# Kernel optimization log

Hardware: AMD Instinct MI355X
Metric: run time of the kernel (lower is better)

Reference implementation:

```python
import jax, jax.numpy as jnp
import numpy as np
import math

D_MODEL = 1024
NUM_HEADS = 16


def setup_inputs() -> dict:
    key = jax.random.key(0)
    kx, kq, kk, kv, ko = jax.random.split(key, 5)
    std = math.sqrt(2.0 / (D_MODEL + D_MODEL))
    def w(k):
        return (jax.random.truncated_normal(k, -3.0, 3.0, (D_MODEL, D_MODEL), jnp.float32) * std)
    return {
        "x": jax.random.normal(kx, (2, 2048, D_MODEL), jnp.float32),
        "Wq": w(kq),
        "Wk": w(kk),
        "Wv": w(kv),
        "Wo": w(ko),
    }


def reference(x, Wq, Wk, Wv, Wo):
    B, S, D = x.shape
    H = NUM_HEADS
    dh = D // H
    # projections: weight is (d_out, d_in)
    def proj(t, W):
        y = jnp.einsum('bsd,ed->bse', t, W)
        return y.reshape(B, S, H, dh).transpose(0, 2, 1, 3)  # b h s dh
    Q = proj(x, Wq)
    K = proj(x, Wk)
    V = proj(x, Wv)
    scale = 1.0 / math.sqrt(dh)
    logits = jnp.einsum('bhqd,bhkd->bhqk', Q, K) * scale
    mask = jnp.tril(jnp.ones((S, S), dtype=bool))  # causal
    logits = jnp.where(mask, logits, -jnp.inf)
    weights = jax.nn.softmax(logits, axis=-1)
    attn = jnp.einsum('bhqk,bhkd->bhqd', weights, V)
    attn = attn.transpose(0, 2, 1, 3).reshape(B, S, D)
    return jnp.einsum('bsd,ed->bse', attn, Wo)
```

## Files before the change

kernel.cpp:

```cpp
#include <hip/hip_runtime.h>
#include <hip/hip_bf16.h>

typedef __bf16 bf16x8 __attribute__((ext_vector_type(8)));
typedef float  f32x4  __attribute__((ext_vector_type(4)));
typedef float  f32x16 __attribute__((ext_vector_type(16)));
typedef unsigned short u16x8 __attribute__((ext_vector_type(8)));
typedef unsigned short u16x4 __attribute__((ext_vector_type(4)));
typedef unsigned int   u32x4 __attribute__((ext_vector_type(4)));

#define WAITV(N) asm volatile("s_waitcnt vmcnt(" #N ")" ::: "memory")
#define SBAR()   do { __builtin_amdgcn_s_barrier(); asm volatile("" ::: "memory"); } while (0)


__device__ __forceinline__ unsigned short f2bf(float f) {
  return __builtin_bit_cast(unsigned short, (__bf16)f);
}

__device__ __forceinline__ bf16x8 ld8(const unsigned short* p) {
  return __builtin_bit_cast(bf16x8, *reinterpret_cast<const u16x8*>(p));
}

__device__ __forceinline__ unsigned int cvtpk(float a, float b) {
  unsigned int r;
  asm("v_cvt_pk_bf16_f32 %0, %1, %2" : "=v"(r) : "v"(a), "v"(b));
  return r;
}

__device__ __forceinline__ float e2(float x) {
  float r;
  asm("v_exp_f32 %0, %1" : "=v"(r) : "v"(x));
  return r;
}

__device__ __forceinline__ void gload16(const unsigned short* src, unsigned short* lds) {
  __builtin_amdgcn_global_load_lds(
      (const __attribute__((address_space(1))) unsigned int*)src,
      (__attribute__((address_space(3))) unsigned int*)lds,
      16, 0, 0);
}


__global__ __launch_bounds__(256) void cvt_inputs(
    const float* __restrict__ x, const float* __restrict__ Wq,
    const float* __restrict__ Wk, const float* __restrict__ Wv,
    const float* __restrict__ Wo,
    unsigned short* __restrict__ xb, unsigned short* __restrict__ wb) {
  const int NXC = 4194304 / 8;
  const int NWC = 1048576 / 8;
  const int total = NXC + 4 * NWC;
  for (int cid = blockIdx.x * 256 + threadIdx.x; cid < total; cid += gridDim.x * 256) {
    const float* s; unsigned short* d; int off;
    if (cid < NXC) { s = x; d = xb; off = cid * 8; }
    else {
      const int c2 = cid - NXC; const int w = c2 >> 17; const int o2 = c2 & (NWC - 1);
      s = (w == 0) ? Wq : (w == 1) ? Wk : (w == 2) ? Wv : Wo;
      d = wb + (size_t)w * 1048576;
      off = o2 * 8;
    }
    const f32x4 a  = *reinterpret_cast<const f32x4*>(s + off);
    const f32x4 b2 = *reinterpret_cast<const f32x4*>(s + off + 4);
    u16x8 o;
#pragma unroll
    for (int j = 0; j < 4; ++j) { o[j] = f2bf(a[j]); o[j + 4] = f2bf(b2[j]); }
    *reinterpret_cast<u16x8*>(d + off) = o;
  }
}


template<int BM>
__device__ __forceinline__ void gemm_body(const unsigned short* __restrict__ A,
                                          const unsigned short* __restrict__ W,
                                          void* __restrict__ Cv, int mode) {
  constexpr int FM  = BM / 32;
  constexpr int WTM = BM / 2;
  __shared__ unsigned short As[2][BM * 64];
  __shared__ unsigned short Bs[2][64 * 64];
  const int tid  = threadIdx.x;
  const int lane = tid & 63;
  const int g    = lane >> 4;
  const int lo   = lane & 15;
  const int wid  = tid >> 6;
  const int m0   = blockIdx.y * BM;
  const int n0   = blockIdx.x * 64;
  const int wm   = wid >> 1, wn = wid & 1;

  f32x4 acc[FM][2] = {};

  auto stage = [&](int buf, int k0) {
#pragma unroll
    for (int i = 0; i < BM / 32; ++i) {
      const int c   = i * 256 + tid;
      const int row = c >> 3, cc = c & 7;
      const int scc = cc ^ (row & 7);
      gload16(A + (size_t)(m0 + row) * 1024 + k0 + scc * 8, &As[buf][(i * 4 + wid) * 512]);
    }
#pragma unroll
    for (int i = 0; i < 2; ++i) {
      const int c   = i * 256 + tid;
      const int row = c >> 3, cc = c & 7;
      const int scc = cc ^ (row & 7);
      gload16(W + (size_t)(n0 + row) * 1024 + k0 + scc * 8, &Bs[buf][(i * 4 + wid) * 512]);
    }
  };

  stage(0, 0);
  stage(1, 64);
  int cur = 0;
  for (int t = 0; t < 16; ++t) {
    if (t < 15) {
      if constexpr (BM == 64) WAITV(4); else WAITV(6);
    } else {
      WAITV(0);
    }
    SBAR();
#pragma unroll
    for (int ks = 0; ks < 2; ++ks) {
      const int slot = (ks * 4 + g) ^ (lo & 7);
      bf16x8 af[FM], bvf[2];
#pragma unroll
      for (int mi = 0; mi < FM; ++mi)
        af[mi] = ld8(&As[cur][(wm * WTM + mi * 16 + lo) * 64 + slot * 8]);
#pragma unroll
      for (int ni = 0; ni < 2; ++ni)
        bvf[ni] = ld8(&Bs[cur][(wn * 32 + ni * 16 + lo) * 64 + slot * 8]);
#pragma unroll
      for (int mi = 0; mi < FM; ++mi)
#pragma unroll
        for (int ni = 0; ni < 2; ++ni)
          acc[mi][ni] = __builtin_amdgcn_mfma_f32_16x16x32_bf16(af[mi], bvf[ni], acc[mi][ni], 0, 0, 0);
    }
    SBAR();
    if (t + 2 < 16) stage(cur, (t + 2) * 64);
    cur ^= 1;
  }

#pragma unroll
  for (int mi = 0; mi < FM; ++mi) {
#pragma unroll
    for (int ni = 0; ni < 2; ++ni) {
      const int gcol = n0 + wn * 32 + ni * 16 + lo;
      if (mode == 2) {
        const int s0 = m0 + wm * WTM + mi * 16 + g * 4;
        const int b = s0 >> 11, s = s0 & 2047;
        const int h = gcol >> 6, d = gcol & 63;
        u16x4 pk;
#pragma unroll
        for (int r = 0; r < 4; ++r) pk[r] = f2bf(acc[mi][ni][r]);
        *reinterpret_cast<u16x4*>(
            &((unsigned short*)Cv)[(((size_t)(b * 16 + h)) * 64 + d) * 2048 + s]) = pk;
      } else {
#pragma unroll
        for (int r = 0; r < 4; ++r) {
          const int grow = m0 + wm * WTM + mi * 16 + g * 4 + r;
          if (mode == 0) {
            ((float*)Cv)[(size_t)grow * 1024 + gcol] = acc[mi][ni][r];
          } else {
            const unsigned short bv = f2bf(acc[mi][ni][r]);
            const int b = grow >> 11, s = grow & 2047;
            const int h = gcol >> 6, d = gcol & 63;
            ((unsigned short*)Cv)[(((size_t)(b * 16 + h)) * 2048 + s) * 64 + d] = bv;
          }
        }
      }
    }
  }
}

__global__ __launch_bounds__(256) void gemm_qkv(
    const unsigned short* __restrict__ xb,
    const unsigned short* __restrict__ wb,
    unsigned short* __restrict__ q_s,
    unsigned short* __restrict__ k_s,
    unsigned short* __restrict__ vt_s) {
  const unsigned short* W = wb + (size_t)blockIdx.z * 1048576;
  void* o; int mode;
  if (blockIdx.z == 0)      { o = q_s;  mode = 1; }
  else if (blockIdx.z == 1) { o = k_s;  mode = 1; }
  else                      { o = vt_s; mode = 2; }
  gemm_body<64>(xb, W, o, mode);
}

__global__ __launch_bounds__(256) void gemm_out(
    const unsigned short* __restrict__ a_s,
    const unsigned short* __restrict__ wb,
    float* __restrict__ out) {
  gemm_body<64>(a_s, wb + (size_t)3 * 1048576, out, 0);
}


__global__ __launch_bounds__(512, 4) void attn_fwd(
    const unsigned short* __restrict__ Q,
    const unsigned short* __restrict__ K,
    const unsigned short* __restrict__ Vt,
    unsigned short* __restrict__ O) {
  __shared__ unsigned short Kl[2][128 * 64];
  __shared__ unsigned short Vl[2][2][64 * 64];
  const int tid  = threadIdx.x;
  const int lane = tid & 63;
  const int wid  = tid >> 6;
  const int qs   = wid & 3;
  const int kh   = wid >> 2;
  const int q31  = lane & 31;
  const int hi   = lane >> 5;
  const int bi   = blockIdx.x;
  const int bh   = bi & 31;
  const int j    = (bi < 256) ? (15 - (bi >> 5)) : ((bi - 256) >> 5);
  const int b    = bh >> 4, h = bh & 15;

  const unsigned short* Qb = Q  + (size_t)bh * 2048 * 64;
  const unsigned short* Kb = K  + (size_t)bh * 2048 * 64;
  const unsigned short* Vb = Vt + (size_t)bh * 64 * 2048;
  const float SC = 0.125f * 1.4426950408889634f;

  auto stage = [&](int buf, int t) {
#pragma unroll
    for (int i = 0; i < 2; ++i) {
      const int c   = i * 512 + tid;
      const int row = c >> 3, cc = c & 7;
      const int scc = cc ^ (row & 7);
      gload16(Kb + (size_t)(t * 128 + row) * 64 + scc * 8, &Kl[buf][(i * 8 + wid) * 512]);
    }
#pragma unroll
    for (int i = 0; i < 2; ++i) {
      const int d  = tid >> 3, cc = tid & 7;
      const int scc = cc ^ (d & 7);
      gload16(Vb + (size_t)d * 2048 + t * 128 + i * 64 + scc * 8, &Vl[buf][i][wid * 512]);
    }
  };

  const int R  = j + 1;
  const int qv = j * 128 + qs * 32 + q31;

  bf16x8 qf[4];
#pragma unroll
  for (int ds = 0; ds < 4; ++ds) {
    bf16x8 tq = ld8(Qb + (size_t)qv * 64 + ds * 16 + hi * 8);
#pragma unroll
    for (int jx = 0; jx < 8; ++jx) tq[jx] = (__bf16)((float)tq[jx] * SC);
    qf[ds] = tq;
  }

  f32x16 oacc[2] = {};
  float m = -1.0e30f;
  float l = 0.f;

  stage(0, 0);
  int buf = 0;

  for (int t = 0; t < R; ++t) {
    SBAR();
    if (t + 1 < R) { stage(buf ^ 1, t + 1); WAITV(4); }
    else WAITV(0);
    SBAR();

    const bool lastt = (t == j);
    const bool skipw = lastt && (kh == 1) && (qs < 2);
    if (!skipw) {
      f32x16 sv[2];
      __builtin_amdgcn_s_setprio(1);
#pragma unroll
      for (int kt2 = 0; kt2 < 2; ++kt2) {
        const int row = kh * 64 + kt2 * 32 + q31;
        f32x16 a = {};
#pragma unroll
        for (int ds = 0; ds < 4; ++ds) {
          bf16x8 kf = ld8(&Kl[buf][row * 64 + ((ds * 2 + hi) ^ (row & 7)) * 8]);
          a = __builtin_amdgcn_mfma_f32_32x32x16_bf16(kf, qf[ds], a, 0, 0, 0);
        }
        sv[kt2] = a;
      }
      __builtin_amdgcn_s_setprio(0);

      const bool domask = lastt && !(kh == 0 && qs >= 2);
      float t0 = -1.0e30f, t1 = -1.0e30f, t2 = -1.0e30f, t3 = -1.0e30f;
      if (domask) {
#pragma unroll
        for (int kt2 = 0; kt2 < 2; ++kt2)
#pragma unroll
          for (int r = 0; r < 16; ++r) {
            float v = sv[kt2][r];
            const int key = t * 128 + kh * 64 + kt2 * 32 + (r & 3) + 8 * (r >> 2) + 4 * hi;
            if (key > qv) v = -INFINITY;
            sv[kt2][r] = v;
            if ((r & 3) == 0) t0 = fmaxf(t0, v);
            else if ((r & 3) == 1) t1 = fmaxf(t1, v);
            else if ((r & 3) == 2) t2 = fmaxf(t2, v);
            else t3 = fmaxf(t3, v);
          }
      } else {
#pragma unroll
        for (int kt2 = 0; kt2 < 2; ++kt2)
#pragma unroll
          for (int r = 0; r < 16; ++r) {
            const float v = sv[kt2][r];
            if ((r & 3) == 0) t0 = fmaxf(t0, v);
            else if ((r & 3) == 1) t1 = fmaxf(t1, v);
            else if ((r & 3) == 2) t2 = fmaxf(t2, v);
            else t3 = fmaxf(t3, v);
          }
      }
      const float tmax = fmaxf(fmaxf(t0, t1), fmaxf(t2, t3));

      if (!__all(tmax <= m + 8.f)) {
        float rmax = fmaxf(tmax, __shfl_xor(tmax, 32));
        const float mn   = fmaxf(m, rmax);
        const float corr = e2(m - mn);
        l *= corr;
#pragma unroll
        for (int dt = 0; dt < 2; ++dt)
#pragma unroll
          for (int r = 0; r < 16; ++r) oacc[dt][r] *= corr;
        m = mn;
      }

      float p0 = 0.f, p1 = 0.f, p2 = 0.f, p3 = 0.f;
#pragma unroll
      for (int kt2 = 0; kt2 < 2; ++kt2)
#pragma unroll
        for (int r = 0; r < 16; ++r) {
          const float p = e2(sv[kt2][r] - m);
          sv[kt2][r] = p;
          if ((r & 3) == 0) p0 += p;
          else if ((r & 3) == 1) p1 += p;
          else if ((r & 3) == 2) p2 += p;
          else p3 += p;
        }
      l += (p0 + p1) + (p2 + p3);

      unsigned int pw[4][4];
#pragma unroll
      for (int ks = 0; ks < 4; ++ks) {
        const int kt2 = ks >> 1, Rr = (ks & 1) * 8;
        unsigned int a0 = cvtpk(sv[kt2][Rr + 0], sv[kt2][Rr + 1]);
        unsigned int c0 = cvtpk(sv[kt2][Rr + 4], sv[kt2][Rr + 5]);
        unsigned int a1 = cvtpk(sv[kt2][Rr + 2], sv[kt2][Rr + 3]);
        unsigned int c1 = cvtpk(sv[kt2][Rr + 6], sv[kt2][Rr + 7]);
        asm("v_permlane32_swap_b32 %0, %1" : "+v"(a0), "+v"(c0));
        asm("v_permlane32_swap_b32 %0, %1" : "+v"(a1), "+v"(c1));
        pw[ks][0] = a0; pw[ks][1] = a1; pw[ks][2] = c0; pw[ks][3] = c1;
      }

      __builtin_amdgcn_s_setprio(1);
#pragma unroll
      for (int dt = 0; dt < 2; ++dt) {
        const int dl = dt * 32 + q31;
#pragma unroll
        for (int ks = 0; ks < 4; ++ks) {
          bf16x8 vfr = ld8(&Vl[buf][kh][dl * 64 + ((ks * 2 + hi) ^ (dl & 7)) * 8]);
          u32x4 t4 = {pw[ks][0], pw[ks][1], pw[ks][2], pw[ks][3]};
          bf16x8 pb = __builtin_bit_cast(bf16x8, t4);
          oacc[dt] = __builtin_amdgcn_mfma_f32_32x32x16_bf16(vfr, pb, oacc[dt], 0, 0, 0);
        }
      }
      __builtin_amdgcn_s_setprio(0);
    }

    buf ^= 1;
  }

  SBAR();
  float* VlF = (float*)&Vl[0][0][0];
  float* KlF = (float*)&Kl[0][0];
  const int mi = qs * 64 + lane;
  if (kh == 1) {
    *reinterpret_cast<f32x16*>(&VlF[mi * 32])      = oacc[0];
    *reinterpret_cast<f32x16*>(&VlF[mi * 32 + 16]) = oacc[1];
    KlF[mi * 2] = m; KlF[mi * 2 + 1] = l;
  }
  SBAR();
  if (kh == 0) {
    const f32x16 o1a = *reinterpret_cast<const f32x16*>(&VlF[mi * 32]);
    const f32x16 o1b = *reinterpret_cast<const f32x16*>(&VlF[mi * 32 + 16]);
    const float m1 = KlF[mi * 2], l1 = KlF[mi * 2 + 1];
    const float mm = fmaxf(m, m1);
    const float c0 = e2(m - mm), c1 = e2(m1 - mm);
    float lr = l * c0 + l1 * c1;
    lr += __shfl_xor(lr, 32);
    const float inv = 1.f / lr;
    const size_t obase = ((size_t)(b * 2048 + qv)) * 1024 + h * 64;
#pragma unroll
    for (int dt = 0; dt < 2; ++dt)
#pragma unroll
      for (int r4 = 0; r4 < 4; ++r4) {
        u16x4 pk;
#pragma unroll
        for (int e = 0; e < 4; ++e) {
          const int r = r4 * 4 + e;
          const float o1 = (dt == 0) ? o1a[r] : o1b[r];
          pk[e] = f2bf((oacc[dt][r] * c0 + o1 * c1) * inv);
        }
        *reinterpret_cast<u16x4*>(&O[obase + dt * 32 + r4 * 8 + hi * 4]) = pk;
      }
  }
}


extern "C" void kernel_launch(void* const* d_in, const int* in_sizes, int n_in,
                              void* d_out, int out_size, void* d_ws, size_t ws_size,
                              hipStream_t stream) {
  const float* x  = (const float*)d_in[0];
  const float* Wq = (const float*)d_in[1];
  const float* Wk = (const float*)d_in[2];
  const float* Wv = (const float*)d_in[3];
  const float* Wo = (const float*)d_in[4];
  float* out = (float*)d_out;

  char* ws = (char*)d_ws;
  const size_t MiB = 1024 * 1024;
  unsigned short* x_bf = (unsigned short*)(ws);
  unsigned short* a_s  = (unsigned short*)(ws);
  unsigned short* w_bf = (unsigned short*)(ws + 8  * MiB);
  unsigned short* q_s  = (unsigned short*)(ws + 16 * MiB);
  unsigned short* k_s  = (unsigned short*)(ws + 24 * MiB);
  unsigned short* vt_s = (unsigned short*)(ws + 32 * MiB);

  cvt_inputs<<<2048, dim3(256), 0, stream>>>(x, Wq, Wk, Wv, Wo, x_bf, w_bf);
  gemm_qkv<<<dim3(16, 64, 3), dim3(256), 0, stream>>>(x_bf, w_bf, q_s, k_s, vt_s);
  attn_fwd<<<512, dim3(512), 0, stream>>>(q_s, k_s, vt_s, a_s);
  gemm_out<<<dim3(16, 64, 1), dim3(256), 0, stream>>>(a_s, w_bf, out);
}
```

Baseline: 105.0 us.

## Enlarge projection GEMM tiles and switch to 32x32x16 MFMA with BK=32

Reworks the projection GEMMs to use larger block tiles (128x128 for QKV, 64x128 for output) with a K-step of 32 and the 32x32x16 bf16 MFMA. LDS layout and swizzle are changed to match, and the epilogue is remapped for the 32x32 accumulator layout. The goal is more data reuse per load and fewer LDS reads per MFMA. In exchange there are fewer blocks, twice as many K iterations with barriers, and more accumulator registers per thread.

After: 99.85 us. 4.9% less time.

```diff
diff --git a/kernel.cpp b/kernel.cpp
--- a/kernel.cpp
+++ b/kernel.cpp
@@ -67,91 +67,97 @@
 }
 
 
-template<int BM>
+template<int BM, int BN>
 __device__ __forceinline__ void gemm_body(const unsigned short* __restrict__ A,
                                           const unsigned short* __restrict__ W,
                                           void* __restrict__ Cv, int mode) {
-  constexpr int FM  = BM / 32;
+  constexpr int FM2 = BM / 64;
+  constexpr int NF2 = BN / 64;
   constexpr int WTM = BM / 2;
-  __shared__ unsigned short As[2][BM * 64];
-  __shared__ unsigned short Bs[2][64 * 64];
+  constexpr int WTN = BN / 2;
+  __shared__ unsigned short As[2][BM * 32];
+  __shared__ unsigned short Bs[2][BN * 32];
   const int tid  = threadIdx.x;
   const int lane = tid & 63;
-  const int g    = lane >> 4;
-  const int lo   = lane & 15;
+  const int q31  = lane & 31;
+  const int hi   = lane >> 5;
   const int wid  = tid >> 6;
   const int m0   = blockIdx.y * BM;
-  const int n0   = blockIdx.x * 64;
+  const int n0   = blockIdx.x * BN;
   const int wm   = wid >> 1, wn = wid & 1;
 
-  f32x4 acc[FM][2] = {};
+  f32x16 acc[FM2][NF2] = {};
 
   auto stage = [&](int buf, int k0) {
 #pragma unroll
-    for (int i = 0; i < BM / 32; ++i) {
+    for (int i = 0; i < BM / 64; ++i) {
       const int c   = i * 256 + tid;
-      const int row = c >> 3, cc = c & 7;
-      const int scc = cc ^ (row & 7);
+      const int row = c >> 2, cc = c & 3;
+      const int scc = cc ^ ((row >> 1) & 3);
       gload16(A + (size_t)(m0 + row) * 1024 + k0 + scc * 8, &As[buf][(i * 4 + wid) * 512]);
     }
 #pragma unroll
-    for (int i = 0; i < 2; ++i) {
+    for (int i = 0; i < BN / 64; ++i) {
       const int c   = i * 256 + tid;
-      const int row = c >> 3, cc = c & 7;
-      const int scc = cc ^ (row & 7);
+      const int row = c >> 2, cc = c & 3;
+      const int scc = cc ^ ((row >> 1) & 3);
       gload16(W + (size_t)(n0 + row) * 1024 + k0 + scc * 8, &Bs[buf][(i * 4 + wid) * 512]);
     }
   };
 
   stage(0, 0);
-  stage(1, 64);
+  stage(1, 32);
   int cur = 0;
-  for (int t = 0; t < 16; ++t) {
-    if (t < 15) {
-      if constexpr (BM == 64) WAITV(4); else WAITV(6);
+  for (int t = 0; t < 32; ++t) {
+    if (t < 31) {
+      if constexpr (BM / 64 + BN / 64 == 4) WAITV(4); else WAITV(3);
     } else {
       WAITV(0);
     }
     SBAR();
 #pragma unroll
     for (int ks = 0; ks < 2; ++ks) {
-      const int slot = (ks * 4 + g) ^ (lo & 7);
-      bf16x8 af[FM], bvf[2];
-#pragma unroll
-      for (int mi = 0; mi < FM; ++mi)
-        af[mi] = ld8(&As[cur][(wm * WTM + mi * 16 + lo) * 64 + slot * 8]);
-#pragma unroll
-      for (int ni = 0; ni < 2; ++ni)
-        bvf[ni] = ld8(&Bs[cur][(wn * 32 + ni * 16 + lo) * 64 + slot * 8]);
-#pragma unroll
-      for (int mi = 0; mi < FM; ++mi)
-#pragma unroll
-        for (int ni = 0; ni < 2; ++ni)
-          acc[mi][ni] = __builtin_amdgcn_mfma_f32_16x16x32_bf16(af[mi], bvf[ni], acc[mi][ni], 0, 0, 0);
+      const int slot = (2 * ks + hi) ^ ((q31 >> 1) & 3);
+      bf16x8 af[FM2], bvf[NF2];
+#pragma unroll
+      for (int mi = 0; mi < FM2; ++mi)
+        af[mi] = ld8(&As[cur][(wm * WTM + mi * 32 + q31) * 32 + slot * 8]);
+#pragma unroll
+      for (int ni = 0; ni < NF2; ++ni)
+        bvf[ni] = ld8(&Bs[cur][(wn * WTN + ni * 32 + q31) * 32 + slot * 8]);
+#pragma unroll
+      for (int mi = 0; mi < FM2; ++mi)
+#pragma unroll
+        for (int ni = 0; ni < NF2; ++ni)
+          acc[mi][ni] = __builtin_amdgcn_mfma_f32_32x32x16_bf16(af[mi], bvf[ni], acc[mi][ni], 0, 0, 0);
     }
     SBAR();
-    if (t + 2 < 16) stage(cur, (t + 2) * 64);
+    if (t + 2 < 32) stage(cur, (t + 2) * 32);
     cur ^= 1;
   }
 
 #pragma unroll
-  for (int mi = 0; mi < FM; ++mi) {
-#pragma unroll
-    for (int ni = 0; ni < 2; ++ni) {
-      const int gcol = n0 + wn * 32 + ni * 16 + lo;
+  for (int mi = 0; mi < FM2; ++mi) {
+#pragma unroll
+    for (int ni = 0; ni < NF2; ++ni) {
+      const int gcol  = n0 + wn * WTN + ni * 32 + q31;
+      const int gbase = m0 + wm * WTM + mi * 32;
       if (mode == 2) {
-        const int s0 = m0 + wm * WTM + mi * 16 + g * 4;
-        const int b = s0 >> 11, s = s0 & 2047;
         const int h = gcol >> 6, d = gcol & 63;
-        u16x4 pk;
-#pragma unroll
-        for (int r = 0; r < 4; ++r) pk[r] = f2bf(acc[mi][ni][r]);
-        *reinterpret_cast<u16x4*>(
-            &((unsigned short*)Cv)[(((size_t)(b * 16 + h)) * 64 + d) * 2048 + s]) = pk;
+#pragma unroll
+        for (int r4 = 0; r4 < 4; ++r4) {
+          const int s0 = gbase + r4 * 8 + hi * 4;
+          const int b = s0 >> 11, s = s0 & 2047;
+          u16x4 pk;
+#pragma unroll
+          for (int e = 0; e < 4; ++e) pk[e] = f2bf(acc[mi][ni][r4 * 4 + e]);
+          *reinterpret_cast<u16x4*>(
+              &((unsigned short*)Cv)[(((size_t)(b * 16 + h)) * 64 + d) * 2048 + s]) = pk;
+        }
       } else {
 #pragma unroll
-        for (int r = 0; r < 4; ++r) {
-          const int grow = m0 + wm * WTM + mi * 16 + g * 4 + r;
+        for (int r = 0; r < 16; ++r) {
+          const int grow = gbase + (r & 3) + 8 * (r >> 2) + 4 * hi;
           if (mode == 0) {
             ((float*)Cv)[(size_t)grow * 1024 + gcol] = acc[mi][ni][r];
           } else {
@@ -166,7 +172,7 @@
   }
 }
 
-__global__ __launch_bounds__(256) void gemm_qkv(
+__global__ __launch_bounds__(256, 4) void gemm_qkv(
     const unsigned short* __restrict__ xb,
     const unsigned short* __restrict__ wb,
     unsigned short* __restrict__ q_s,
@@ -177,14 +183,14 @@
   if (blockIdx.z == 0)      { o = q_s;  mode = 1; }
   else if (blockIdx.z == 1) { o = k_s;  mode = 1; }
   else                      { o = vt_s; mode = 2; }
-  gemm_body<64>(xb, W, o, mode);
-}
-
-__global__ __launch_bounds__(256) void gemm_out(
+  gemm_body<128, 128>(xb, W, o, mode);
+}
+
+__global__ __launch_bounds__(256, 4) void gemm_out(
     const unsigned short* __restrict__ a_s,
     const unsigned short* __restrict__ wb,
     float* __restrict__ out) {
-  gemm_body<64>(a_s, wb + (size_t)3 * 1048576, out, 0);
+  gemm_body<64, 128>(a_s, wb + (size_t)3 * 1048576, out, 0);
 }
 
 
@@ -415,7 +421,7 @@
   unsigned short* vt_s = (unsigned short*)(ws + 32 * MiB);
 
   cvt_inputs<<<2048, dim3(256), 0, stream>>>(x, Wq, Wk, Wv, Wo, x_bf, w_bf);
-  gemm_qkv<<<dim3(16, 64, 3), dim3(256), 0, stream>>>(x_bf, w_bf, q_s, k_s, vt_s);
+  gemm_qkv<<<dim3(8, 32, 3), dim3(256), 0, stream>>>(x_bf, w_bf, q_s, k_s, vt_s);
   attn_fwd<<<512, dim3(512), 0, stream>>>(q_s, k_s, vt_s, a_s);
-  gemm_out<<<dim3(16, 64, 1), dim3(256), 0, stream>>>(a_s, w_bf, out);
-}
+  gemm_out<<<dim3(8, 64, 1), dim3(256), 0, stream>>>(a_s, w_bf, out);
+}
```
